# Kernel optimization log

Hardware: AMD Instinct MI355X
Metric: run time of the kernel (lower is better)

Reference implementation:

```python
import jax, jax.numpy as jnp
import numpy as np

BN_EPS = 1e-5


def setup_inputs() -> dict:
    key = jax.random.key(0)
    k1, k2, k3, k4, k5 = jax.random.split(key, 5)
    B, N, K, C_in, C_out = 8, 8192, 16, 64, 64
    x = jax.random.normal(k1, (B, N, C_in), dtype=jnp.float32)
    knn = jax.random.randint(k2, (B, N, K), 0, N, dtype=jnp.int64)
    # learned params: linear weight (out, in), BN affine params.
    # NOTE: module inits bn.weight to `init`=0.0 which would zero the output;
    # we use random gamma so the baseline exercises nontrivial math.
    W = jax.random.normal(k3, (C_out, C_in), dtype=jnp.float32) * (1.0 / np.sqrt(C_in))
    gamma = jax.random.normal(k4, (C_out,), dtype=jnp.float32) * 0.1 + 1.0
    beta = jax.random.normal(k5, (C_out,), dtype=jnp.float32) * 0.1
    return {"x": x, "knn": knn, "W": W, "gamma": gamma, "beta": beta}


def reference(x, knn, W, gamma, beta):
    B, N, C = x.shape
    # linear projection (no bias): [B,N,C_in] x [C_out,C_in] -> [B,N,C_out]
    h = jnp.einsum('bnc,oc->bno', x, W)
    # KNN gather + mean aggregation: agg[b,n] = mean_k h[b, knn[b,n,k]]
    agg = jax.vmap(lambda hb, kb: hb[kb])(h, knn).mean(axis=2)  # [B,N,C_out]
    # BatchNorm1d in training mode over B*N tokens (biased variance)
    flat = agg.reshape(B * N, -1)
    mu = flat.mean(axis=0)
    var = flat.var(axis=0)
    out = (flat - mu) * jax.lax.rsqrt(var + BN_EPS) * gamma + beta
    return out.reshape(B, N, -1)
```

## Files before the change

### kernel.cpp

```cpp
#include <hip/hip_runtime.h>

#define BB 8
#define NN 8192
#define KK 16
#define CC 64
#define TPB 64
#define THREADS 256
#define BPB (NN / TPB)
#define NBLK (BB * BPB)
#define NTOK (BB * NN)
#define BN_EPS 1e-5f

__global__ __launch_bounds__(THREADS) void k_fused_gather(
    const float* __restrict__ x, const int* __restrict__ knn,
    const float* __restrict__ W, float* __restrict__ agg,
    float* __restrict__ partials)
{
    __shared__ float sWt[CC][CC];
    __shared__ float sAgg[TPB][CC + 4];
    __shared__ float sRed[2][16][CC];

    const int tid   = threadIdx.x;
    const int batch = blockIdx.x & 7;
    const int chunk = blockIdx.x >> 3;
    const int n_base = chunk * TPB;

    for (int i = tid; i < CC * CC; i += THREADS) {
        const int o = i >> 6, c = i & 63;
        sWt[c][o] = W[i];
    }

    const int g = tid >> 4;
    const int l = tid & 15;
    const float4* __restrict__ x4 = (const float4*)x;

    for (int it = 0; it < TPB / 16; ++it) {
        const int t = it * 16 + g;
        const int n = n_base + t;
        const int idx_my = knn[(batch * NN + n) * KK + l];
        float sx = 0.f, sy = 0.f, sz = 0.f, sw = 0.f;
        #pragma unroll
        for (int k = 0; k < KK; ++k) {
            const int idx = __shfl(idx_my, k, 16);
            const float4 v = x4[(size_t)(batch * NN + idx) * (CC / 4) + l];
            sx += v.x; sy += v.y; sz += v.z; sw += v.w;
        }
        const float inv = 1.0f / KK;
        *(float4*)&sAgg[t][l * 4] = make_float4(sx * inv, sy * inv, sz * inv, sw * inv);
    }
    __syncthreads();

    const int tq = tid >> 4;
    const int oq = tid & 15;
    float acc[4][4] = {};
    #pragma unroll
    for (int c4 = 0; c4 < CC; c4 += 4) {
        float av[4][4], wv[4][4];
        #pragma unroll
        for (int t = 0; t < 4; ++t) {
            const float4 tmp = *(const float4*)&sAgg[tq * 4 + t][c4];
            av[t][0] = tmp.x; av[t][1] = tmp.y; av[t][2] = tmp.z; av[t][3] = tmp.w;
        }
        #pragma unroll
        for (int cc = 0; cc < 4; ++cc) {
            const float4 tmp = *(const float4*)&sWt[c4 + cc][oq * 4];
            wv[cc][0] = tmp.x; wv[cc][1] = tmp.y; wv[cc][2] = tmp.z; wv[cc][3] = tmp.w;
        }
        #pragma unroll
        for (int t = 0; t < 4; ++t)
            #pragma unroll
            for (int cc = 0; cc < 4; ++cc)
                #pragma unroll
                for (int o = 0; o < 4; ++o)
                    acc[t][o] += av[t][cc] * wv[cc][o];
    }

    float4* __restrict__ agg4 = (float4*)agg;
    float ps[4] = {}, pq[4] = {};
    #pragma unroll
    for (int t = 0; t < 4; ++t) {
        const int n = n_base + tq * 4 + t;
        agg4[(size_t)(batch * NN + n) * (CC / 4) + oq] =
            make_float4(acc[t][0], acc[t][1], acc[t][2], acc[t][3]);
        #pragma unroll
        for (int o = 0; o < 4; ++o) {
            ps[o] += acc[t][o];
            pq[o] += acc[t][o] * acc[t][o];
        }
    }
    #pragma unroll
    for (int o = 0; o < 4; ++o) {
        sRed[0][tq][oq * 4 + o] = ps[o];
        sRed[1][tq][oq * 4 + o] = pq[o];
    }
    __syncthreads();
    if (tid < 128) {
        const int w = tid >> 6, c = tid & 63;
        float s = 0.f;
        #pragma unroll
        for (int i = 0; i < 16; ++i) s += sRed[w][i][c];
        partials[blockIdx.x * 128 + tid] = s;
    }
}

__global__ __launch_bounds__(128) void k_reduce1(
    const float* __restrict__ partials, float* __restrict__ p2)
{
    const int tid = threadIdx.x;
    const int j = blockIdx.x;
    float s = 0.f;
    #pragma unroll
    for (int i = 0; i < NBLK / 64; ++i)
        s += partials[(size_t)(j * (NBLK / 64) + i) * 128 + tid];
    p2[j * 128 + tid] = s;
}

__global__ __launch_bounds__(128) void k_stats(
    const float* __restrict__ p2, const float* __restrict__ gamma,
    const float* __restrict__ beta, float* __restrict__ ss)
{
    __shared__ float tot[128];
    const int tid = threadIdx.x;
    float s = 0.f;
    #pragma unroll
    for (int j = 0; j < 64; ++j) s += p2[j * 128 + tid];
    tot[tid] = s;
    __syncthreads();
    if (tid < CC) {
        const float invn = 1.0f / (float)NTOK;
        const float mu  = tot[tid] * invn;
        const float var = tot[64 + tid] * invn - mu * mu;
        const float sc  = gamma[tid] * rsqrtf(var + BN_EPS);
        ss[tid]      = sc;
        ss[CC + tid] = beta[tid] - mu * sc;
    }
}

__global__ __launch_bounds__(256) void k_norm(
    float* __restrict__ out, const float* __restrict__ ss)
{
    const int idx = blockIdx.x * 256 + threadIdx.x;
    const float4 a  = ((const float4*)out)[idx];
    const int c4 = idx & (CC / 4 - 1);
    const float4 sc = ((const float4*)ss)[c4];
    const float4 sh = ((const float4*)ss)[CC / 4 + c4];
    ((float4*)out)[idx] = make_float4(
        fmaf(a.x, sc.x, sh.x), fmaf(a.y, sc.y, sh.y),
        fmaf(a.z, sc.z, sh.z), fmaf(a.w, sc.w, sh.w));
}

extern "C" void kernel_launch(void* const* d_in, const int* in_sizes, int n_in,
                              void* d_out, int out_size, void* d_ws, size_t ws_size,
                              hipStream_t stream)
{
    const float* x     = (const float*)d_in[0];
    const int*   knn   = (const int*)d_in[1];
    const float* W     = (const float*)d_in[2];
    const float* gamma = (const float*)d_in[3];
    const float* beta  = (const float*)d_in[4];
    float* out = (float*)d_out;

    float* partials = (float*)d_ws;
    float* p2       = partials + NBLK * 128;
    float* ss       = p2 + 64 * 128;

    k_fused_gather<<<NBLK, THREADS, 0, stream>>>(x, knn, W, out, partials);
    k_reduce1<<<64, 128, 0, stream>>>(partials, p2);
    k_stats<<<1, 128, 0, stream>>>(p2, gamma, beta, ss);
    k_norm<<<out_size / 4 / 256, 256, 0, stream>>>(out, ss);
}
```

Before: 39.46 us.

## Batch gather loads, share LDS buffers, merge stats reductions, nontemporal stores

The gather loop now shuffles out all 16 neighbor indices first and issues all 16 vector loads before a tree reduction, so more memory requests are in flight. The aggregation and reduction shared buffers are unioned to cut LDS use, and launch bounds request higher occupancy. The two-stage stats reduction is merged into one 64-block kernel using wave shuffles, removing a launch. Index loads and the final output stores use nontemporal hints. The extra barrier and higher register pressure from 16 live vectors may offset some of this.

Measured after the change: 41.62 us. 5.5% more time.

```diff
diff --git a/kernel.cpp b/kernel.cpp
--- a/kernel.cpp
+++ b/kernel.cpp
@@ -1,4 +1,6 @@
 #include <hip/hip_runtime.h>
+
+typedef float f4 __attribute__((ext_vector_type(4)));
 
 #define BB 8
 #define NN 8192
@@ -6,64 +8,59 @@
 #define CC 64
 #define TPB 64
 #define THREADS 256
-#define BPB (NN / TPB)
-#define NBLK (BB * BPB)
+#define NCHUNK 1024
 #define NTOK (BB * NN)
 #define BN_EPS 1e-5f
 
-__global__ __launch_bounds__(THREADS) void k_fused_gather(
+__global__ __launch_bounds__(THREADS, 4) void k_main(
     const float* __restrict__ x, const int* __restrict__ knn,
-    const float* __restrict__ W, float* __restrict__ agg,
+    const float* __restrict__ W, float* __restrict__ out,
     float* __restrict__ partials)
 {
     __shared__ float sWt[CC][CC];
-    __shared__ float sAgg[TPB][CC + 4];
-    __shared__ float sRed[2][16][CC];
+    __shared__ union { float agg[TPB][CC + 4]; float red[2][16][CC]; } u;
 
     const int tid   = threadIdx.x;
     const int batch = blockIdx.x & 7;
-    const int chunk = blockIdx.x >> 3;
-    const int n_base = chunk * TPB;
+    const int nb    = (blockIdx.x >> 3) * TPB;
 
-    for (int i = tid; i < CC * CC; i += THREADS) {
-        const int o = i >> 6, c = i & 63;
-        sWt[c][o] = W[i];
-    }
+    for (int i = tid; i < CC * CC; i += THREADS)
+        sWt[i & 63][i >> 6] = W[i];
 
-    const int g = tid >> 4;
-    const int l = tid & 15;
-    const float4* __restrict__ x4 = (const float4*)x;
+    const int g = tid >> 4, l = tid & 15;
+    const f4* __restrict__ x4b = (const f4*)x + (size_t)batch * NN * (CC / 4);
 
-    for (int it = 0; it < TPB / 16; ++it) {
+    for (int it = 0; it < 4; ++it) {
         const int t = it * 16 + g;
-        const int n = n_base + t;
-        const int idx_my = knn[(batch * NN + n) * KK + l];
-        float sx = 0.f, sy = 0.f, sz = 0.f, sw = 0.f;
+        const int idx_my =
+            __builtin_nontemporal_load(&knn[(batch * NN + nb + t) * KK + l]);
+        int idxs[16];
         #pragma unroll
-        for (int k = 0; k < KK; ++k) {
-            const int idx = __shfl(idx_my, k, 16);
-            const float4 v = x4[(size_t)(batch * NN + idx) * (CC / 4) + l];
-            sx += v.x; sy += v.y; sz += v.z; sw += v.w;
-        }
-        const float inv = 1.0f / KK;
-        *(float4*)&sAgg[t][l * 4] = make_float4(sx * inv, sy * inv, sz * inv, sw * inv);
+        for (int k = 0; k < KK; ++k) idxs[k] = __shfl(idx_my, k, 16);
+        f4 v[16];
+        #pragma unroll
+        for (int k = 0; k < KK; ++k) v[k] = x4b[idxs[k] * (CC / 4) + l];
+        #pragma unroll
+        for (int s = 8; s; s >>= 1)
+            #pragma unroll
+            for (int k = 0; k < s; ++k) v[k] += v[k + s];
+        *(f4*)&u.agg[t][l * 4] = v[0] * (1.0f / KK);
     }
     __syncthreads();
 
-    const int tq = tid >> 4;
-    const int oq = tid & 15;
+    const int tq = tid >> 4, oq = tid & 15;
     float acc[4][4] = {};
     #pragma unroll
     for (int c4 = 0; c4 < CC; c4 += 4) {
         float av[4][4], wv[4][4];
         #pragma unroll
         for (int t = 0; t < 4; ++t) {
-            const float4 tmp = *(const float4*)&sAgg[tq * 4 + t][c4];
+            const f4 tmp = *(const f4*)&u.agg[tq * 4 + t][c4];
             av[t][0] = tmp.x; av[t][1] = tmp.y; av[t][2] = tmp.z; av[t][3] = tmp.w;
         }
         #pragma unroll
         for (int cc = 0; cc < 4; ++cc) {
-            const float4 tmp = *(const float4*)&sWt[c4 + cc][oq * 4];
+            const f4 tmp = *(const f4*)&sWt[c4 + cc][oq * 4];
             wv[cc][0] = tmp.x; wv[cc][1] = tmp.y; wv[cc][2] = tmp.z; wv[cc][3] = tmp.w;
         }
         #pragma unroll
@@ -75,64 +72,65 @@
                     acc[t][o] += av[t][cc] * wv[cc][o];
     }
 
-    float4* __restrict__ agg4 = (float4*)agg;
+    f4* __restrict__ out4 = (f4*)out;
+    #pragma unroll
+    for (int t = 0; t < 4; ++t) {
+        f4 r; r.x = acc[t][0]; r.y = acc[t][1]; r.z = acc[t][2]; r.w = acc[t][3];
+        out4[(size_t)(batch * NN + nb + tq * 4 + t) * (CC / 4) + oq] = r;
+    }
+
+    __syncthreads();
     float ps[4] = {}, pq[4] = {};
     #pragma unroll
-    for (int t = 0; t < 4; ++t) {
-        const int n = n_base + tq * 4 + t;
-        agg4[(size_t)(batch * NN + n) * (CC / 4) + oq] =
-            make_float4(acc[t][0], acc[t][1], acc[t][2], acc[t][3]);
+    for (int t = 0; t < 4; ++t)
         #pragma unroll
         for (int o = 0; o < 4; ++o) {
             ps[o] += acc[t][o];
             pq[o] += acc[t][o] * acc[t][o];
         }
-    }
     #pragma unroll
     for (int o = 0; o < 4; ++o) {
-        sRed[0][tq][oq * 4 + o] = ps[o];
-        sRed[1][tq][oq * 4 + o] = pq[o];
+        u.red[0][tq][oq * 4 + o] = ps[o];
+        u.red[1][tq][oq * 4 + o] = pq[o];
     }
     __syncthreads();
     if (tid < 128) {
         const int w = tid >> 6, c = tid & 63;
         float s = 0.f;
         #pragma unroll
-        for (int i = 0; i < 16; ++i) s += sRed[w][i][c];
-        partials[blockIdx.x * 128 + tid] = s;
+        for (int i = 0; i < 16; ++i) s += u.red[w][i][c];
+        partials[(size_t)blockIdx.x * 128 + tid] = s;
     }
 }
 
-__global__ __launch_bounds__(128) void k_reduce1(
-    const float* __restrict__ partials, float* __restrict__ p2)
+__global__ __launch_bounds__(THREADS) void k_stats(
+    const float* __restrict__ partials, const float* __restrict__ gamma,
+    const float* __restrict__ beta, float* __restrict__ ss)
 {
+    __shared__ float sFin[8];
     const int tid = threadIdx.x;
     const int j = blockIdx.x;
-    float s = 0.f;
+    float s1 = 0.f, s2 = 0.f;
+    for (int i = tid; i < NCHUNK; i += THREADS) {
+        s1 += partials[(size_t)i * 128 + j];
+        s2 += partials[(size_t)i * 128 + 64 + j];
+    }
     #pragma unroll
-    for (int i = 0; i < NBLK / 64; ++i)
-        s += partials[(size_t)(j * (NBLK / 64) + i) * 128 + tid];
-    p2[j * 128 + tid] = s;
-}
-
-__global__ __launch_bounds__(128) void k_stats(
-    const float* __restrict__ p2, const float* __restrict__ gamma,
-    const float* __restrict__ beta, float* __restrict__ ss)
-{
-    __shared__ float tot[128];
-    const int tid = threadIdx.x;
-    float s = 0.f;
-    #pragma unroll
-    for (int j = 0; j < 64; ++j) s += p2[j * 128 + tid];
-    tot[tid] = s;
+    for (int off = 32; off; off >>= 1) {
+        s1 += __shfl_down(s1, off);
+        s2 += __shfl_down(s2, off);
+    }
+    if ((tid & 63) == 0) { sFin[tid >> 6] = s1; sFin[4 + (tid >> 6)] = s2; }
     __syncthreads();
-    if (tid < CC) {
+    if (tid == 0) {
+        const float S1 = sFin[0] + sFin[1] + sFin[2] + sFin[3];
+        const float S2 = sFin[4] + sFin[5] + sFin[6] + sFin[7];
         const float invn = 1.0f / (float)NTOK;
-        const float mu  = tot[tid] * invn;
-        const float var = tot[64 + tid] * invn - mu * mu;
-        const float sc  = gamma[tid] * rsqrtf(var + BN_EPS);
-        ss[tid]      = sc;
-        ss[CC + tid] = beta[tid] - mu * sc;
+        const float mu  = S1 * invn;
+        const float var = S2 * invn - mu * mu;
+        const float sc  = gamma[j] * rsqrtf(var + BN_EPS);
+        ss[j]      = sc;
+        ss[CC + j] = beta[j] - mu * sc;
     }
 }
 
@@ -140,13 +138,17 @@
     float* __restrict__ out, const float* __restrict__ ss)
 {
     const int idx = blockIdx.x * 256 + threadIdx.x;
-    const float4 a  = ((const float4*)out)[idx];
+    f4* out4 = (f4*)out;
+    const f4 a  = out4[idx];
     const int c4 = idx & (CC / 4 - 1);
-    const float4 sc = ((const float4*)ss)[c4];
-    const float4 sh = ((const float4*)ss)[CC / 4 + c4];
-    ((float4*)out)[idx] = make_float4(
-        fmaf(a.x, sc.x, sh.x), fmaf(a.y, sc.y, sh.y),
-        fmaf(a.z, sc.z, sh.z), fmaf(a.w, sc.w, sh.w));
+    const f4 sc = ((const f4*)ss)[c4];
+    const f4 sh = ((const f4*)ss)[CC / 4 + c4];
+    f4 r;
+    r.x = fmaf(a.x, sc.x, sh.x);
+    r.y = fmaf(a.y, sc.y, sh.y);
+    r.z = fmaf(a.z, sc.z, sh.z);
+    r.w = fmaf(a.w, sc.w, sh.w);
+    __builtin_nontemporal_store(r, &out4[idx]);
 }
 
 extern "C" void kernel_launch(void* const* d_in, const int* in_sizes, int n_in,
@@ -161,11 +163,9 @@
     float* out = (float*)d_out;
 
     float* partials = (float*)d_ws;
-    float* p2       = partials + NBLK * 128;
-    float* ss       = p2 + 64 * 128;
+    float* ss       = partials + NCHUNK * 128;
 
-    k_fused_gather<<<NBLK, THREADS, 0, stream>>>(x, knn, W, out, partials);
-    k_reduce1<<<64, 128, 0, stream>>>(partials, p2);
-    k_stats<<<1, 128, 0, stream>>>(p2, gamma, beta, ss);
-    k_norm<<<out_size / 4 / 256, 256, 0, stream>>>(out, ss);
+    k_main <<<NCHUNK, THREADS, 0, stream>>>(x, knn, W, out, partials);
+    k_stats<<<64, THREADS, 0, stream>>>(partials, gamma, beta, ss);
+    k_norm <<<(NTOK * CC) / 4 / 256, 256, 0, stream>>>(out, ss);
 }
```
